# Performance work log

Hardware: AMD Instinct MI355X
Metric: run time of the kernel (lower is better)

## Reference

```python
import jax, jax.numpy as jnp
import numpy as np

D_MODEL = 1024
N_HEADS = 16
HEAD_DIM = D_MODEL // N_HEADS


def setup_inputs() -> dict:
    key = jax.random.key(0)
    ks = jax.random.split(key, 9)
    s = 1.0 / np.sqrt(D_MODEL)
    x = jax.random.normal(ks[0], (2, 2048, D_MODEL), dtype=jnp.float32)
    Wq = jax.random.uniform(ks[1], (D_MODEL, D_MODEL), jnp.float32, -s, s)
    bq = jax.random.uniform(ks[2], (D_MODEL,), jnp.float32, -s, s)
    Wk = jax.random.uniform(ks[3], (D_MODEL, D_MODEL), jnp.float32, -s, s)
    bk = jax.random.uniform(ks[4], (D_MODEL,), jnp.float32, -s, s)
    Wv = jax.random.uniform(ks[5], (D_MODEL, D_MODEL), jnp.float32, -s, s)
    bv = jax.random.uniform(ks[6], (D_MODEL,), jnp.float32, -s, s)
    Wo = jax.random.uniform(ks[7], (D_MODEL, D_MODEL), jnp.float32, -s, s)
    bo = jax.random.uniform(ks[8], (D_MODEL,), jnp.float32, -s, s)
    return {"x": x, "Wq": Wq, "bq": bq, "Wk": Wk, "bk": bk,
            "Wv": Wv, "bv": bv, "Wo": Wo, "bo": bo}


def reference(x, Wq, bq, Wk, bk, Wv, bv, Wo, bo):
    B, S, _ = x.shape
    # project and split heads: [B, H, S, Dh]
    def heads(W, b):
        return (x @ W + b).reshape(B, S, N_HEADS, HEAD_DIM).transpose(0, 2, 1, 3)
    Q, K, V = heads(Wq, bq), heads(Wk, bk), heads(Wv, bv)
    scale = 1.0 / np.sqrt(HEAD_DIM).astype(np.float32)
    scores = jnp.einsum('bhsd,bhtd->bhst', Q, K) * scale  # [B,H,S,S]
    causal = jnp.tril(jnp.ones((S, S), dtype=bool))
    scores = jnp.where(causal, scores, -jnp.inf)
    attn = jax.nn.softmax(scores, axis=-1)
    out = jnp.einsum('bhst,bhtd->bhsd', attn, V)  # [B,H,S,Dh]
    out = out.transpose(0, 2, 1, 3).reshape(B, S, D_MODEL)
    return out @ Wo + bo
```

## Files before the change

kernel.cpp:

```cpp
#include <hip/hip_runtime.h>

typedef __attribute__((ext_vector_type(8))) __bf16 bfrag;
typedef __attribute__((ext_vector_type(4))) float f32x4;

#define MFMA(a, b, c) __builtin_amdgcn_mfma_f32_16x16x32_bf16((a), (b), (c), 0, 0, 0)

#define D_MODEL 1024
#define SEQ     2048
#define NB      2
#define NH      16
#define HD      64
#define MROWS   (NB * SEQ)

#define SCALE_LOG2 0.18033688011112043f
#define NEG_BIG    (-3.0e38f)

#define GLOBAL_AS(p) ((const __attribute__((address_space(1))) void*)(p))
#define LDS_AS(p)    ((__attribute__((address_space(3))) void*)(p))
#define ASYNC_CP16(g, l) __builtin_amdgcn_global_load_lds(GLOBAL_AS(g), LDS_AS(l), 16, 0, 0)

__global__ __launch_bounds__(256) void k_prep(
    const float* __restrict__ x,
    const float* __restrict__ Wq, const float* __restrict__ Wk,
    const float* __restrict__ Wv, const float* __restrict__ Wo,
    __bf16* __restrict__ Wt, __bf16* __restrict__ xb)
{
    __shared__ __bf16 t[64][65];
    if (blockIdx.z == 4) {
        size_t base = ((size_t)(blockIdx.y * 16 + blockIdx.x)) * 16384;
        for (int j = 0; j < 8; ++j) {
            size_t i = base + (size_t)j * 2048 + (size_t)threadIdx.x * 8;
            float4 f0 = *(const float4*)&x[i];
            float4 f1 = *(const float4*)&x[i + 4];
            union { uint4 u; __bf16 h[8]; } cv;
            cv.h[0] = (__bf16)f0.x; cv.h[1] = (__bf16)f0.y;
            cv.h[2] = (__bf16)f0.z; cv.h[3] = (__bf16)f0.w;
            cv.h[4] = (__bf16)f1.x; cv.h[5] = (__bf16)f1.y;
            cv.h[6] = (__bf16)f1.z; cv.h[7] = (__bf16)f1.w;
            *(uint4*)&xb[i] = cv.u;
        }
        return;
    }
    const float* src = (blockIdx.z == 0) ? Wq : (blockIdx.z == 1) ? Wk
                      : (blockIdx.z == 2) ? Wv : Wo;
    __bf16* dst = Wt + (size_t)blockIdx.z * (1024u * 1024u);
    int tr = blockIdx.y * 64, tc = blockIdx.x * 64;
    for (int j = 0; j < 16; ++j) {
        int id = threadIdx.x + j * 256;
        int r = id >> 6, c = id & 63;
        t[r][c] = (__bf16)src[(size_t)(tr + r) * 1024 + tc + c];
    }
    __syncthreads();
    for (int j = 0; j < 16; ++j) {
        int id = threadIdx.x + j * 256;
        int r = id >> 6, c = id & 63;
        dst[(size_t)(tc + r) * 1024 + tr + c] = t[c][r];
    }
}

template <int MODE, bool WT>
__global__ __launch_bounds__(256) void k_gemm128(
    const void* __restrict__ Ap,
    const void* __restrict__ W0, const void* __restrict__ W1,
    const void* __restrict__ W2,
    const float* __restrict__ b0, const float* __restrict__ b1,
    const float* __restrict__ b2, void* __restrict__ dstp)
{
    constexpr int AST = WT ? 64 : 72;
    alignas(16) __shared__ __bf16 SH[18432];
    __bf16* As = SH;
    __bf16* Bs = SH + 128 * AST;

    const int tid = threadIdx.x;
    const int z = blockIdx.z;
    const int m0 = blockIdx.y * 128;
    const int n0 = blockIdx.x * 128;
    const void* W     = (z == 0) ? W0 : (z == 1) ? W1 : W2;
    const float* bias = (z == 0) ? b0 : (z == 1) ? b1 : b2;

    const int wid = tid >> 6, lane = tid & 63;
    const int quad = lane >> 4, l16 = lane & 15;
    const int wRow = (wid >> 1) * 64, wCol = (wid & 1) * 64;

    f32x4 acc[4][4];
    const f32x4 zero = {0.f, 0.f, 0.f, 0.f};
    for (int mi = 0; mi < 4; ++mi)
        for (int ni = 0; ni < 4; ++ni) acc[mi][ni] = zero;

    const int srow = tid >> 3;
    const int sseg = (tid & 7) * 8;
    const int bkrow = tid >> 4;
    const int bnseg = (tid & 15) * 8;
    const int arow = lane >> 3;
    const int akoff = ((lane & 7) * 8) ^ (arow * 8);
    const int sw = (l16 & 7) * 8;

    for (int k0 = 0; k0 < D_MODEL; k0 += 64) {
        __syncthreads();
        if (WT) {
            const __bf16* Ab = (const __bf16*)Ap;
            const __bf16* Bt = (const __bf16*)W;
            for (int it = 0; it < 4; ++it) {
                int row = wid * 32 + it * 8;
                ASYNC_CP16(&Ab[(size_t)(m0 + row + arow) * D_MODEL + k0 + akoff],
                           &As[row * 64]);
                ASYNC_CP16(&Bt[(size_t)(n0 + row + arow) * D_MODEL + k0 + akoff],
                           &Bs[row * 64]);
            }
        } else {
            if (MODE == 0) {
                const float* A = (const float*)Ap;
                for (int it = 0; it < 4; ++it) {
                    int row = srow + it * 32;
                    const float* src = &A[(size_t)(m0 + row) * D_MODEL + k0 + sseg];
                    float4 f0 = *(const float4*)src;
                    float4 f1 = *(const float4*)(src + 4);
                    union { uint4 u; __bf16 h[8]; } cv;
                    cv.h[0] = (__bf16)f0.x; cv.h[1] = (__bf16)f0.y;
                    cv.h[2] = (__bf16)f0.z; cv.h[3] = (__bf16)f0.w;
                    cv.h[4] = (__bf16)f1.x; cv.h[5] = (__bf16)f1.y;
                    cv.h[6] = (__bf16)f1.z; cv.h[7] = (__bf16)f1.w;
                    *(uint4*)&As[row * AST + sseg] = cv.u;
                }
            } else {
                const __bf16* A = (const __bf16*)Ap;
                for (int it = 0; it < 4; ++it) {
                    int row = srow + it * 32;
                    uint4 va = *(const uint4*)&A[(size_t)(m0 + row) * D_MODEL + k0 + sseg];
                    *(uint4*)&As[row * AST + sseg] = va;
                }
            }
            const float* Wf = (const float*)W;
            for (int it = 0; it < 4; ++it) {
                int krow = bkrow + it * 16;
                const float* src = &Wf[(size_t)(k0 + krow) * D_MODEL + n0 + bnseg];
                float4 f0 = *(const float4*)src;
                float4 f1 = *(const float4*)(src + 4);
                Bs[(bnseg + 0) * AST + krow] = (__bf16)f0.x;
                Bs[(bnseg + 1) * AST + krow] = (__bf16)f0.y;
                Bs[(bnseg + 2) * AST + krow] = (__bf16)f0.z;
                Bs[(bnseg + 3) * AST + krow] = (__bf16)f0.w;
                Bs[(bnseg + 4) * AST + krow] = (__bf16)f1.x;
                Bs[(bnseg + 5) * AST + krow] = (__bf16)f1.y;
                Bs[(bnseg + 6) * AST + krow] = (__bf16)f1.z;
                Bs[(bnseg + 7) * AST + krow] = (__bf16)f1.w;
            }
        }
        __syncthreads();
        for (int kk = 0; kk < 64; kk += 32) {
            bfrag af[4], bf[4];
            if (WT) {
                int ko = (kk + quad * 8) ^ sw;
                for (int mi = 0; mi < 4; ++mi)
                    af[mi] = *(const bfrag*)&As[(wRow + mi * 16 + l16) * 64 + ko];
                for (int ni = 0; ni < 4; ++ni)
                    bf[ni] = *(const bfrag*)&Bs[(wCol + ni * 16 + l16) * 64 + ko];
            } else {
                for (int mi = 0; mi < 4; ++mi)
                    af[mi] = *(const bfrag*)&As[(wRow + mi * 16 + l16) * AST + kk + quad * 8];
                for (int ni = 0; ni < 4; ++ni)
                    bf[ni] = *(const bfrag*)&Bs[(wCol + ni * 16 + l16) * AST + kk + quad * 8];
            }
            for (int mi = 0; mi < 4; ++mi)
                for (int ni = 0; ni < 4; ++ni)
                    acc[mi][ni] = MFMA(af[mi], bf[ni], acc[mi][ni]);
        }
    }

    if (MODE == 0) {
        float biasv[4];
        for (int ni = 0; ni < 4; ++ni) biasv[ni] = bias[n0 + wCol + ni * 16 + l16];
        const int b = m0 >> 11, m0s = m0 & 2047, h0 = n0 >> 6;
        __syncthreads();
        if (z < 2) {
            for (int mi = 0; mi < 4; ++mi)
                for (int ni = 0; ni < 4; ++ni) {
                    int col = wCol + ni * 16 + l16;
                    for (int r = 0; r < 4; ++r) {
                        float v = acc[mi][ni][r] + biasv[ni];
                        if (z == 0) v *= SCALE_LOG2;
                        SH[(wRow + mi * 16 + quad * 4 + r) * 136 + col] = (__bf16)v;
                    }
                }
            __syncthreads();
            __bf16* qk = (__bf16*)dstp + (size_t)z * (MROWS * (size_t)D_MODEL);
            for (int i = 0; i < 8; ++i) {
                int rid = i * 32 + (tid >> 3);
                int hl = rid >> 7, sl = rid & 127;
                int dcol = (tid & 7) * 8;
                uint4 v = *(const uint4*)&SH[sl * 136 + hl * 64 + dcol];
                *(uint4*)&qk[(((size_t)b * NH + h0 + hl) * SEQ + m0s + sl) * HD + dcol] = v;
            }
        } else {
            for (int mi = 0; mi < 4; ++mi)
                for (int ni = 0; ni < 4; ++ni) {
                    int col = wCol + ni * 16 + l16;
                    int s0 = wRow + mi * 16 + quad * 4;
                    union { unsigned long long u; __bf16 h4[4]; } pk;
                    for (int r = 0; r < 4; ++r)
                        pk.h4[r] = (__bf16)(acc[mi][ni][r] + biasv[ni]);
                    *(unsigned long long*)&SH[col * 136 + s0] = pk.u;
                }
            __syncthreads();
            __bf16* vv = (__bf16*)dstp + (size_t)2 * (MROWS * (size_t)D_MODEL);
            for (int i = 0; i < 8; ++i) {
                int rid = i * 16 + (tid >> 4);
                int hl = rid >> 6, d = rid & 63;
                int sc = (tid & 15) * 8;
                uint4 v = *(const uint4*)&SH[rid * 136 + sc];
                *(uint4*)&vv[(((size_t)b * NH + h0 + hl) * HD + d) * SEQ + m0s + sc] = v;
            }
        }
    } else {
        for (int mi = 0; mi < 4; ++mi)
            for (int ni = 0; ni < 4; ++ni) {
                int gn = n0 + wCol + ni * 16 + l16;
                float bv = bias[gn];
                for (int r = 0; r < 4; ++r) {
                    int gm = m0 + wRow + mi * 16 + quad * 4 + r;
                    ((float*)dstp)[(size_t)gm * D_MODEL + gn] = acc[mi][ni][r] + bv;
                }
            }
    }
}

__global__ __launch_bounds__(256) void k_attn(
    const __bf16* __restrict__ Q, const __bf16* __restrict__ K,
    const __bf16* __restrict__ Vt, __bf16* __restrict__ O)
{
    alignas(16) __shared__ __bf16 Ks[64 * 72];
    alignas(16) __shared__ __bf16 Vts[64 * 72];
    alignas(16) __shared__ __bf16 Ps[4][16 * 72];

    const int tid = threadIdx.x, wid = tid >> 6, lane = tid & 63;
    const int quad = lane >> 4, l16 = lane & 15;
    const int qb = (blockIdx.x + blockIdx.y + 16 * blockIdx.z) & 31;
    const int h = blockIdx.y, b = blockIdx.z;
    const size_t bh = ((size_t)b * NH + h) * SEQ * HD;
    const __bf16* Qg  = Q + bh + (size_t)qb * 64 * HD;
    const __bf16* Kg  = K + bh;
    const __bf16* Vtg = Vt + ((size_t)b * NH + h) * HD * SEQ;

    bfrag qf[2];
    qf[0] = *(const bfrag*)&Qg[(size_t)(wid * 16 + l16) * HD + quad * 8];
    qf[1] = *(const bfrag*)&Qg[(size_t)(wid * 16 + l16) * HD + 32 + quad * 8];

    const f32x4 zero = {0.f, 0.f, 0.f, 0.f};
    f32x4 o[4];
    for (int dt = 0; dt < 4; ++dt) o[dt] = zero;
    float mrow = NEG_BIG, lrow = 0.f;
    const int q = qb * 64 + wid * 16 + l16;
    const int srcbase = (lane & 48) + quad * 4;
    const int ntile = qb + 1;

    const int row0 = tid >> 3, seg = (tid & 7) * 8;

    uint4 kreg0 = *(const uint4*)&Kg[(size_t)row0 * HD + seg];
    uint4 kreg1 = *(const uint4*)&Kg[(size_t)(row0 + 32) * HD + seg];
    uint4 vreg0 = *(const uint4*)&Vtg[(size_t)row0 * SEQ + seg];
    uint4 vreg1 = *(const uint4*)&Vtg[(size_t)(row0 + 32) * SEQ + seg];

    for (int t = 0; t < ntile; ++t) {
        const int j0 = t * 64;
        __syncthreads();
        *(uint4*)&Ks[row0 * 72 + seg] = kreg0;
        *(uint4*)&Ks[(row0 + 32) * 72 + seg] = kreg1;
        *(uint4*)&Vts[row0 * 72 + seg] = vreg0;
        *(uint4*)&Vts[(row0 + 32) * 72 + seg] = vreg1;
        if (t + 1 < ntile) {
            const int j1 = j0 + 64;
            kreg0 = *(const uint4*)&Kg[(size_t)(j1 + row0) * HD + seg];
            kreg1 = *(const uint4*)&Kg[(size_t)(j1 + row0 + 32) * HD + seg];
            vreg0 = *(const uint4*)&Vtg[(size_t)row0 * SEQ + j1 + seg];
            vreg1 = *(const uint4*)&Vtg[(size_t)(row0 + 32) * SEQ + j1 + seg];
        }
        __syncthreads();

        f32x4 st[4];
        for (int kt = 0; kt < 4; ++kt) {
            bfrag ka0 = *(const bfrag*)&Ks[(kt * 16 + l16) * 72 + quad * 8];
            bfrag ka1 = *(const bfrag*)&Ks[(kt * 16 + l16) * 72 + 32 + quad * 8];
            st[kt] = MFMA(ka1, qf[1], MFMA(ka0, qf[0], zero));
        }

        float mloc = NEG_BIG;
        if (t == ntile - 1) {
            for (int kt = 0; kt < 4; ++kt)
                for (int r = 0; r < 4; ++r) {
                    float v = (j0 + kt * 16 + quad * 4 + r > q) ? NEG_BIG : st[kt][r];
                    st[kt][r] = v;
                    mloc = fmaxf(mloc, v);
                }
        } else {
            for (int kt = 0; kt < 4; ++kt)
                for (int r = 0; r < 4; ++r) mloc = fmaxf(mloc, st[kt][r]);
        }
        float m2 = fmaxf(mloc, __shfl_xor(mloc, 16, 64));
        m2 = fmaxf(m2, __shfl_xor(m2, 32, 64));
        float mnew = fmaxf(mrow, m2);
        float alpha = exp2f(mrow - mnew);
        mrow = mnew;
        float sloc = 0.f;
        for (int kt = 0; kt < 4; ++kt)
            for (int r = 0; r < 4; ++r) {
                float p = exp2f(st[kt][r] - mnew);
                st[kt][r] = p;
                sloc += p;
            }

        for (int kt = 0; kt < 4; ++kt) {
            union { unsigned long long u; __bf16 h4[4]; } pk;
            for (int r = 0; r < 4; ++r) pk.h4[r] = (__bf16)st[kt][r];
            *(unsigned long long*)&Ps[wid][l16 * 72 + kt * 16 + quad * 4] = pk.u;
        }

        for (int r = 0; r < 4; ++r) {
            float ar = __shfl(alpha, srcbase + r, 64);
            for (int dt = 0; dt < 4; ++dt) o[dt][r] *= ar;
        }
        asm volatile("s_waitcnt lgkmcnt(0)" ::: "memory");

        for (int c = 0; c < 2; ++c) {
            bfrag pf = *(const bfrag*)&Ps[wid][l16 * 72 + c * 32 + quad * 8];
            for (int dt = 0; dt < 4; ++dt) {
                bfrag vf = *(const bfrag*)&Vts[(dt * 16 + l16) * 72 + c * 32 + quad * 8];
                o[dt] = MFMA(pf, vf, o[dt]);
            }
        }

        float s2 = sloc + __shfl_xor(sloc, 16, 64);
        s2 = s2 + __shfl_xor(s2, 32, 64);
        lrow = alpha * lrow + s2;
    }

    for (int r = 0; r < 4; ++r) {
        float lr = __shfl(lrow, srcbase + r, 64);
        float inv = 1.0f / lr;
        size_t base = ((size_t)b * SEQ + qb * 64 + wid * 16 + quad * 4 + r) * D_MODEL
                    + (size_t)h * HD;
        for (int dt = 0; dt < 4; ++dt)
            O[base + dt * 16 + l16] = (__bf16)(o[dt][r] * inv);
    }
}

extern "C" void kernel_launch(void* const* d_in, const int* in_sizes, int n_in,
                              void* d_out, int out_size, void* d_ws, size_t ws_size,
                              hipStream_t stream)
{
    const float* x  = (const float*)d_in[0];
    const float* Wq = (const float*)d_in[1];
    const float* bq = (const float*)d_in[2];
    const float* Wk = (const float*)d_in[3];
    const float* bk = (const float*)d_in[4];
    const float* Wv = (const float*)d_in[5];
    const float* bv = (const float*)d_in[6];
    const float* Wo = (const float*)d_in[7];
    const float* bo = (const float*)d_in[8];

    __bf16* ws = (__bf16*)d_ws;
    const size_t M1 = 1024u * 1024u;
    __bf16* qkv    = ws;
    __bf16* attn_o = ws + 12 * M1;
    __bf16* Wt     = ws + 16 * M1;
    __bf16* xb     = ws + 20 * M1;

    const bool fast = ws_size >= (size_t)48 * 1024 * 1024;

    if (fast) {
        k_prep<<<dim3(16, 16, 5), 256, 0, stream>>>(x, Wq, Wk, Wv, Wo, Wt, xb);
        k_gemm128<0, true><<<dim3(8, 32, 3), 256, 0, stream>>>(
            xb, Wt, Wt + M1, Wt + 2 * M1, bq, bk, bv, qkv);
        k_attn<<<dim3(32, 16, 2), 256, 0, stream>>>(
            qkv, qkv + 4 * M1, qkv + 8 * M1, attn_o);
        k_gemm128<1, true><<<dim3(8, 32, 1), 256, 0, stream>>>(
            attn_o, Wt + 3 * M1, Wt + 3 * M1, Wt + 3 * M1, bo, bo, bo, (float*)d_out);
    } else {
        k_gemm128<0, false><<<dim3(8, 32, 3), 256, 0, stream>>>(
            x, Wq, Wk, Wv, bq, bk, bv, qkv);
        k_attn<<<dim3(32, 16, 2), 256, 0, stream>>>(
            qkv, qkv + 4 * M1, qkv + 8 * M1, attn_o);
        k_gemm128<1, false><<<dim3(8, 32, 1), 256, 0, stream>>>(
            attn_o, Wo, Wo, Wo, bo, bo, bo, (float*)d_out);
    }
}
```

Before: 224.8 us.

## Add 64x128 output GEMM, XOR-swizzle attention LDS, and balance causal tile order

Adds a dedicated output-projection GEMM with 64x128 tiles, launched as 512 blocks instead of 256 so more of the GPU's compute units are occupied. It loads tiles asynchronously into XOR-swizzled LDS. The attention kernel replaces its padded 72-stride LDS layout with a 64-stride XOR swizzle to avoid bank conflicts while using less shared memory. It also remaps query-block indices so that short and long causal blocks alternate, which balances work across CUs. The swizzle adds index arithmetic, and the smaller GEMM tile reduces data reuse per block.

```diff
diff --git a/kernel.cpp b/kernel.cpp
--- a/kernel.cpp
+++ b/kernel.cpp
@@ -224,17 +224,78 @@
     }
 }
 
+__global__ __launch_bounds__(256) void k_gemm_out(
+    const __bf16* __restrict__ A, const __bf16* __restrict__ Bt,
+    const float* __restrict__ bias, float* __restrict__ dst)
+{
+    alignas(16) __shared__ __bf16 As[64 * 64];
+    alignas(16) __shared__ __bf16 Bs[128 * 64];
+
+    const int tid = threadIdx.x;
+    const int m0 = blockIdx.y * 64;
+    const int n0 = blockIdx.x * 128;
+    const int wid = tid >> 6, lane = tid & 63;
+    const int quad = lane >> 4, l16 = lane & 15;
+    const int wRow = (wid >> 1) * 32, wCol = (wid & 1) * 64;
+
+    f32x4 acc[2][4];
+    const f32x4 zero = {0.f, 0.f, 0.f, 0.f};
+    for (int mi = 0; mi < 2; ++mi)
+        for (int ni = 0; ni < 4; ++ni) acc[mi][ni] = zero;
+
+    const int arow = lane >> 3;
+    const int akoff = ((lane & 7) * 8) ^ (arow * 8);
+    const int sw = (l16 & 7) * 8;
+
+    for (int k0 = 0; k0 < D_MODEL; k0 += 64) {
+        __syncthreads();
+        for (int it = 0; it < 2; ++it) {
+            int row = wid * 16 + it * 8;
+            ASYNC_CP16(&A[(size_t)(m0 + row + arow) * D_MODEL + k0 + akoff],
+                       &As[row * 64]);
+        }
+        for (int it = 0; it < 4; ++it) {
+            int row = wid * 32 + it * 8;
+            ASYNC_CP16(&Bt[(size_t)(n0 + row + arow) * D_MODEL + k0 + akoff],
+                       &Bs[row * 64]);
+        }
+        __syncthreads();
+        for (int kk = 0; kk < 64; kk += 32) {
+            int ko = (kk + quad * 8) ^ sw;
+            bfrag af[2], bf[4];
+            for (int mi = 0; mi < 2; ++mi)
+                af[mi] = *(const bfrag*)&As[(wRow + mi * 16 + l16) * 64 + ko];
+            for (int ni = 0; ni < 4; ++ni)
+                bf[ni] = *(const bfrag*)&Bs[(wCol + ni * 16 + l16) * 64 + ko];
+            for (int mi = 0; mi < 2; ++mi)
+                for (int ni = 0; ni < 4; ++ni)
+                    acc[mi][ni] = MFMA(af[mi], bf[ni], acc[mi][ni]);
+        }
+    }
+
+    for (int mi = 0; mi < 2; ++mi)
+        for (int ni = 0; ni < 4; ++ni) {
+            int gn = n0 + wCol + ni * 16 + l16;
+            float bv = bias[gn];
+            for (int r = 0; r < 4; ++r) {
+                int gm = m0 + wRow + mi * 16 + quad * 4 + r;
+                dst[(size_t)gm * D_MODEL + gn] = acc[mi][ni][r] + bv;
+            }
+        }
+}
+
 __global__ __launch_bounds__(256) void k_attn(
     const __bf16* __restrict__ Q, const __bf16* __restrict__ K,
     const __bf16* __restrict__ Vt, __bf16* __restrict__ O)
 {
-    alignas(16) __shared__ __bf16 Ks[64 * 72];
-    alignas(16) __shared__ __bf16 Vts[64 * 72];
-    alignas(16) __shared__ __bf16 Ps[4][16 * 72];
+    alignas(16) __shared__ __bf16 Ks[64 * 64];
+    alignas(16) __shared__ __bf16 Vts[64 * 64];
+    alignas(16) __shared__ __bf16 Ps[4][16 * 64];
 
     const int tid = threadIdx.x, wid = tid >> 6, lane = tid & 63;
     const int quad = lane >> 4, l16 = lane & 15;
-    const int qb = (blockIdx.x + blockIdx.y + 16 * blockIdx.z) & 31;
+    const int u = (blockIdx.x + blockIdx.y + 16 * blockIdx.z) & 31;
+    const int qb = (u & 1) ? 31 - (u >> 1) : (u >> 1);
     const int h = blockIdx.y, b = blockIdx.z;
     const size_t bh = ((size_t)b * NH + h) * SEQ * HD;
     const __bf16* Qg  = Q + bh + (size_t)qb * 64 * HD;
@@ -251,9 +312,11 @@
     float mrow = NEG_BIG, lrow = 0.f;
     const int q = qb * 64 + wid * 16 + l16;
     const int srcbase = (lane & 48) + quad * 4;
+    const int sw = (l16 & 7) * 8;
     const int ntile = qb + 1;
 
     const int row0 = tid >> 3, seg = (tid & 7) * 8;
+    const int sseg = seg ^ ((row0 & 7) * 8);
 
     uint4 kreg0 = *(const uint4*)&Kg[(size_t)row0 * HD + seg];
     uint4 kreg1 = *(const uint4*)&Kg[(size_t)(row0 + 32) * HD + seg];
@@ -263,10 +326,10 @@
     for (int t = 0; t < ntile; ++t) {
         const int j0 = t * 64;
         __syncthreads();
-        *(uint4*)&Ks[row0 * 72 + seg] = kreg0;
-        *(uint4*)&Ks[(row0 + 32) * 72 + seg] = kreg1;
-        *(uint4*)&Vts[row0 * 72 + seg] = vreg0;
-        *(uint4*)&Vts[(row0 + 32) * 72 + seg] = vreg1;
+        *(uint4*)&Ks[row0 * 64 + sseg] = kreg0;
+        *(uint4*)&Ks[(row0 + 32) * 64 + sseg] = kreg1;
+        *(uint4*)&Vts[row0 * 64 + sseg] = vreg0;
+        *(uint4*)&Vts[(row0 + 32) * 64 + sseg] = vreg1;
         if (t + 1 < ntile) {
             const int j1 = j0 + 64;
             kreg0 = *(const uint4*)&Kg[(size_t)(j1 + row0) * HD + seg];
@@ -278,8 +341,8 @@
 
         f32x4 st[4];
         for (int kt = 0; kt < 4; ++kt) {
-            bfrag ka0 = *(const bfrag*)&Ks[(kt * 16 + l16) * 72 + quad * 8];
-            bfrag ka1 = *(const bfrag*)&Ks[(kt * 16 + l16) * 72 + 32 + quad * 8];
+            bfrag ka0 = *(const bfrag*)&Ks[(kt * 16 + l16) * 64 + ((quad * 8) ^ sw)];
+            bfrag ka1 = *(const bfrag*)&Ks[(kt * 16 + l16) * 64 + ((32 + quad * 8) ^ sw)];
             st[kt] = MFMA(ka1, qf[1], MFMA(ka0, qf[0], zero));
         }
 
@@ -311,7 +374,7 @@
         for (int kt = 0; kt < 4; ++kt) {
             union { unsigned long long u; __bf16 h4[4]; } pk;
             for (int r = 0; r < 4; ++r) pk.h4[r] = (__bf16)st[kt][r];
-            *(unsigned long long*)&Ps[wid][l16 * 72 + kt * 16 + quad * 4] = pk.u;
+            *(unsigned long long*)&Ps[wid][l16 * 64 + ((kt * 16 + quad * 4) ^ sw)] = pk.u;
         }
 
         for (int r = 0; r < 4; ++r) {
@@ -321,9 +384,10 @@
         asm volatile("s_waitcnt lgkmcnt(0)" ::: "memory");
 
         for (int c = 0; c < 2; ++c) {
-            bfrag pf = *(const bfrag*)&Ps[wid][l16 * 72 + c * 32 + quad * 8];
+            int ko = (c * 32 + quad * 8) ^ sw;
+            bfrag pf = *(const bfrag*)&Ps[wid][l16 * 64 + ko];
             for (int dt = 0; dt < 4; ++dt) {
-                bfrag vf = *(const bfrag*)&Vts[(dt * 16 + l16) * 72 + c * 32 + quad * 8];
+                bfrag vf = *(const bfrag*)&Vts[(dt * 16 + l16) * 64 + ko];
                 o[dt] = MFMA(pf, vf, o[dt]);
             }
         }
@@ -372,8 +436,8 @@
             xb, Wt, Wt + M1, Wt + 2 * M1, bq, bk, bv, qkv);
         k_attn<<<dim3(32, 16, 2), 256, 0, stream>>>(
             qkv, qkv + 4 * M1, qkv + 8 * M1, attn_o);
-        k_gemm128<1, true><<<dim3(8, 32, 1), 256, 0, stream>>>(
-            attn_o, Wt + 3 * M1, Wt + 3 * M1, Wt + 3 * M1, bo, bo, bo, (float*)d_out);
+        k_gemm_out<<<dim3(8, 64), 256, 0, stream>>>(
+            attn_o, Wt + 3 * M1, bo, (float*)d_out);
     } else {
         k_gemm128<0, false><<<dim3(8, 32, 3), 256, 0, stream>>>(
             x, Wq, Wk, Wv, bq, bk, bv, qkv);
```

Measured after the change: 212.5 us. 5.5% less time.
